# Optimization experiments

Hardware: AMD Instinct MI355X
Metric: run time of the kernel (lower is better)

## Reference

```python
import jax, jax.numpy as jnp
import numpy as np

D_IN = 1024
D_OUT = 1024
N_HEADS = 16
D_HEAD = D_OUT // N_HEADS


def setup_inputs() -> dict:
    key = jax.random.key(0)
    ks = jax.random.split(key, 6)
    s = 0.02
    return {
        "x": jax.random.normal(ks[0], (4, 2048, D_IN), dtype=jnp.float32),
        "wq": jax.random.normal(ks[1], (D_IN, D_OUT), dtype=jnp.float32) * s,
        "wk": jax.random.normal(ks[2], (D_IN, D_OUT), dtype=jnp.float32) * s,
        "wv": jax.random.normal(ks[3], (D_IN, D_OUT), dtype=jnp.float32) * s,
        "wo": jax.random.normal(ks[4], (D_OUT, D_OUT), dtype=jnp.float32) * s,
        "bo": jax.random.normal(ks[5], (D_OUT,), dtype=jnp.float32) * s,
    }


def reference(x, wq, wk, wv, wo, bo):
    B, T, _ = x.shape
    # QKV projections (no bias), split into heads: (B, H, T, Dh)
    def split_heads(t):
        return t.reshape(B, T, N_HEADS, D_HEAD).transpose(0, 2, 1, 3)
    q = split_heads(x @ wq)
    k = split_heads(x @ wk)
    v = split_heads(x @ wv)
    # attention scores (B, H, T, T), causal mask, scale by sqrt(d_head)
    scores = jnp.einsum("bhqd,bhkd->bhqk", q, k)
    causal = jnp.tril(jnp.ones((T, T), dtype=bool))
    scores = jnp.where(causal, scores, -jnp.inf)
    attn = jax.nn.softmax(scores / jnp.sqrt(jnp.float32(D_HEAD)), axis=-1)
    # dropout = 0.0 (eval) -> identity
    ctx = jnp.einsum("bhqk,bhkd->bhqd", attn, v)
    ctx = ctx.transpose(0, 2, 1, 3).reshape(B, T, D_OUT)
    return ctx @ wo + bo
```

## Files before the change

kernel.cpp:

```cpp
#include <hip/hip_runtime.h>
#include <stdint.h>


typedef unsigned short u16;
typedef __bf16 bf16x8 __attribute__((ext_vector_type(8)));
typedef float f32x4 __attribute__((ext_vector_type(4)));

__device__ __forceinline__ u16 f2bf(float f) {
  union { float f; unsigned u; } v; v.f = f;
  return (u16)((v.u + 0x7fffu + ((v.u >> 16) & 1u)) >> 16);
}

__device__ __forceinline__ void gl_lds16(const void* g, void* l) {
  __builtin_amdgcn_global_load_lds((__attribute__((address_space(1))) void*)g,
                                   (__attribute__((address_space(3))) void*)l,
                                   16, 0, 0);
}

__global__ __launch_bounds__(256) void conv_x_k(const float* __restrict__ x,
                                                u16* __restrict__ xb) {
  int i = (blockIdx.x * 256 + threadIdx.x) * 4;
  float4 v = *reinterpret_cast<const float4*>(x + i);
  ushort4 o;
  o.x = f2bf(v.x); o.y = f2bf(v.y); o.z = f2bf(v.z); o.w = f2bf(v.w);
  *reinterpret_cast<ushort4*>(xb + i) = o;
}

__global__ __launch_bounds__(256) void conv_w_k(const float* __restrict__ w0,
                                                const float* __restrict__ w1,
                                                const float* __restrict__ w2,
                                                const float* __restrict__ w3,
                                                u16* __restrict__ dst) {
  const float* src = blockIdx.z == 0 ? w0 : blockIdx.z == 1 ? w1
                   : blockIdx.z == 2 ? w2 : w3;
  u16* d = dst + (size_t)blockIdx.z * 1024 * 1024;
  __shared__ float tile[32][33];
  int n0 = blockIdx.x * 32, k0 = blockIdx.y * 32;
  int tx = threadIdx.x & 31, ty = threadIdx.x >> 5;
  #pragma unroll
  for (int r = 0; r < 32; r += 8)
    tile[ty + r][tx] = src[(k0 + ty + r) * 1024 + n0 + tx];
  __syncthreads();
  #pragma unroll
  for (int r = 0; r < 32; r += 8)
    d[(n0 + ty + r) * 1024 + k0 + tx] = f2bf(tile[tx][ty + r]);
}

__global__ __launch_bounds__(256) void gemm_qkv_k(const u16* __restrict__ A,
                                                  const u16* __restrict__ Wt,
                                                  u16* __restrict__ qw,
                                                  u16* __restrict__ kw,
                                                  u16* __restrict__ vtw) {
  __shared__ u16 As[128 * 32];
  __shared__ u16 Bs[128 * 32];
  const int tid = threadIdx.x;
  const int wave = tid >> 6, lane = tid & 63;
  const int quad = lane >> 4, l15 = lane & 15;
  const int m0 = blockIdx.x * 128;
  const int which = blockIdx.y >> 3;
  const int n0 = (blockIdx.y & 7) * 128;
  const u16* Bt = Wt + which * (1024 * 1024);
  const int waveM = (wave >> 1) * 64, waveN = (wave & 1) * 64;

  const f32x4 fz = {0.f, 0.f, 0.f, 0.f};
  f32x4 acc[4][4];
  #pragma unroll
  for (int i = 0; i < 4; i++)
    #pragma unroll
    for (int j = 0; j < 4; j++) acc[i][j] = fz;

  const int grow = tid >> 2, gc8 = (tid & 3) * 8;
  const u16* Ag = A + (m0 + grow) * 1024 + gc8;
  const u16* Bg = Bt + (n0 + grow) * 1024 + gc8;
  char* AsB = (char*)As + wave * 1024;
  char* BsB = (char*)Bs + wave * 1024;

  for (int k0 = 0; k0 < 1024; k0 += 32) {
    __syncthreads();
    gl_lds16(Ag + k0, AsB);
    gl_lds16(Ag + 65536 + k0, AsB + 4096);
    gl_lds16(Bg + k0, BsB);
    gl_lds16(Bg + 65536 + k0, BsB + 4096);
    __syncthreads();
    bf16x8 af[4], bf[4];
    #pragma unroll
    for (int mi = 0; mi < 4; mi++)
      af[mi] = *reinterpret_cast<const bf16x8*>(&As[(waveM + mi * 16 + l15) * 32 + quad * 8]);
    #pragma unroll
    for (int ni = 0; ni < 4; ni++)
      bf[ni] = *reinterpret_cast<const bf16x8*>(&Bs[(waveN + ni * 16 + l15) * 32 + quad * 8]);
    #pragma unroll
    for (int mi = 0; mi < 4; mi++)
      #pragma unroll
      for (int ni = 0; ni < 4; ni++)
        acc[mi][ni] = __builtin_amdgcn_mfma_f32_16x16x32_bf16(af[mi], bf[ni], acc[mi][ni], 0, 0, 0);
  }
  #pragma unroll
  for (int mi = 0; mi < 4; mi++) {
    #pragma unroll
    for (int r = 0; r < 4; r++) {
      int m = m0 + waveM + mi * 16 + quad * 4 + r;
      int b = m >> 11, t = m & 2047;
      #pragma unroll
      for (int ni = 0; ni < 4; ni++) {
        int n = n0 + waveN + ni * 16 + l15;
        int h = n >> 6, d = n & 63;
        float v = acc[mi][ni][r];
        if (which == 0)      qw[((b * 16 + h) * 2048 + t) * 64 + d] = f2bf(v * 0.125f);
        else if (which == 1) kw[((b * 16 + h) * 2048 + t) * 64 + d] = f2bf(v);
        else                 vtw[((b * 16 + h) * 64 + d) * 2048 + t] = f2bf(v);
      }
    }
  }
}

__global__ __launch_bounds__(256) void attn_k(const u16* __restrict__ Q,
                                              const u16* __restrict__ K,
                                              const u16* __restrict__ Vt,
                                              u16* __restrict__ ctx) {
  __shared__ u16 QPs[64 * 64];
  __shared__ u16 Ks[2][64 * 64];
  __shared__ u16 Vs[2][64 * 64];
  const int tid = threadIdx.x;
  const int wave = tid >> 6, lane = tid & 63;
  const int quad = lane >> 4, l15 = lane & 15;
  const int bh = blockIdx.x;
  const int qt = 31 - (int)blockIdx.y;
  const int b = bh >> 4, h = bh & 15;

  const u16* Qg = Q + (bh * 2048 + qt * 64) * 64;
  const u16* Kg = K + bh * (2048 * 64);
  const u16* Vg = Vt + bh * (64 * 2048);

  const int lrow = tid >> 3;
  const int lsw = ((tid & 7) ^ (lrow & 7)) * 8;

  gl_lds16(Qg + lrow * 64 + lsw, (char*)QPs + wave * 1024);
  gl_lds16(Qg + (32 + lrow) * 64 + lsw, (char*)QPs + wave * 1024 + 4096);
  {
    char* KsB = (char*)Ks[0] + wave * 1024;
    char* VsB = (char*)Vs[0] + wave * 1024;
    gl_lds16(Kg + lrow * 64 + lsw, KsB);
    gl_lds16(Kg + (32 + lrow) * 64 + lsw, KsB + 4096);
    gl_lds16(Vg + lrow * 2048 + lsw, VsB);
    gl_lds16(Vg + (32 + lrow) * 2048 + lsw, VsB + 4096);
  }

  bf16x8 onesb;
  #pragma unroll
  for (int i = 0; i < 8; i++) onesb[i] = (__bf16)1.0f;

  const f32x4 fz = {0.f, 0.f, 0.f, 0.f};
  f32x4 accO[4];
  f32x4 accL = fz;
  #pragma unroll
  for (int dt = 0; dt < 4; dt++) accO[dt] = fz;
  bf16x8 qf[2];

  #define SWZB(row, chunk) ((row) * 128 + (((chunk) ^ ((row) & 7)) << 4))

  for (int j = 0; j <= qt; j++) {
    const int cur = j & 1;
    __syncthreads();
    if (j < qt) {
      char* KsB = (char*)Ks[cur ^ 1] + wave * 1024;
      char* VsB = (char*)Vs[cur ^ 1] + wave * 1024;
      const int jr = (j + 1) * 64;
      gl_lds16(Kg + (jr + lrow) * 64 + lsw, KsB);
      gl_lds16(Kg + (jr + 32 + lrow) * 64 + lsw, KsB + 4096);
      gl_lds16(Vg + lrow * 2048 + jr + lsw, VsB);
      gl_lds16(Vg + (32 + lrow) * 2048 + jr + lsw, VsB + 4096);
    }
    if (j == 0) {
      #pragma unroll
      for (int kk = 0; kk < 2; kk++)
        qf[kk] = *reinterpret_cast<const bf16x8*>(
            (char*)QPs + SWZB(wave * 16 + l15, kk * 4 + quad));
    }

    f32x4 s[4];
    #pragma unroll
    for (int nt = 0; nt < 4; nt++) s[nt] = fz;
    #pragma unroll
    for (int kk = 0; kk < 2; kk++)
      #pragma unroll
      for (int nt = 0; nt < 4; nt++) {
        bf16x8 kf = *reinterpret_cast<const bf16x8*>(
            (char*)Ks[cur] + SWZB(nt * 16 + l15, kk * 4 + quad));
        s[nt] = __builtin_amdgcn_mfma_f32_16x16x32_bf16(qf[kk], kf, s[nt], 0, 0, 0);
      }

    if (j == qt) {
      #pragma unroll
      for (int nt = 0; nt < 4; nt++) {
        int col = nt * 16 + l15;
        int row0 = wave * 16 + quad * 4;
        #pragma unroll
        for (int r = 0; r < 4; r++)
          if (col > row0 + r) s[nt][r] = -1e30f;
      }
    }

    #pragma unroll
    for (int nt = 0; nt < 4; nt++)
      #pragma unroll
      for (int r = 0; r < 4; r++) {
        int prow = wave * 16 + quad * 4 + r;
        int pcol = nt * 16 + l15;
        int byte = prow * 128 + ((((pcol >> 3) ^ (prow & 7))) << 4) + (pcol & 7) * 2;
        *(u16*)((char*)QPs + byte) = f2bf(__expf(s[nt][r]));
      }
    __asm__ volatile("s_waitcnt lgkmcnt(0)" ::: "memory");

    #pragma unroll
    for (int kk = 0; kk < 2; kk++) {
      bf16x8 pf = *reinterpret_cast<const bf16x8*>(
          (char*)QPs + SWZB(wave * 16 + l15, kk * 4 + quad));
      accL = __builtin_amdgcn_mfma_f32_16x16x32_bf16(pf, onesb, accL, 0, 0, 0);
      #pragma unroll
      for (int dt = 0; dt < 4; dt++) {
        bf16x8 vf = *reinterpret_cast<const bf16x8*>(
            (char*)Vs[cur] + SWZB(dt * 16 + l15, kk * 4 + quad));
        accO[dt] = __builtin_amdgcn_mfma_f32_16x16x32_bf16(pf, vf, accO[dt], 0, 0, 0);
      }
    }
  }
  #undef SWZB

  float inv[4];
  #pragma unroll
  for (int r = 0; r < 4; r++) inv[r] = 1.0f / accL[r];
  const int trow = qt * 64 + wave * 16 + quad * 4;
  #pragma unroll
  for (int dt = 0; dt < 4; dt++)
    #pragma unroll
    for (int r = 0; r < 4; r++)
      ctx[(b * 2048 + trow + r) * 1024 + h * 64 + dt * 16 + l15] =
          f2bf(accO[dt][r] * inv[r]);
}

__global__ __launch_bounds__(256) void gemm_out_k(const u16* __restrict__ A,
                                                  const u16* __restrict__ Wt,
                                                  const float* __restrict__ bo,
                                                  float* __restrict__ out) {
  __shared__ u16 As[128 * 32];
  __shared__ u16 Bs[128 * 32];
  const int tid = threadIdx.x;
  const int wave = tid >> 6, lane = tid & 63;
  const int quad = lane >> 4, l15 = lane & 15;
  const int m0 = blockIdx.x * 128;
  const int n0 = blockIdx.y * 128;
  const int waveM = (wave >> 1) * 64, waveN = (wave & 1) * 64;

  const f32x4 fz = {0.f, 0.f, 0.f, 0.f};
  f32x4 acc[4][4];
  #pragma unroll
  for (int i = 0; i < 4; i++)
    #pragma unroll
    for (int j = 0; j < 4; j++) acc[i][j] = fz;

  const int grow = tid >> 2, gc8 = (tid & 3) * 8;
  const u16* Ag = A + (m0 + grow) * 1024 + gc8;
  const u16* Bg = Wt + (n0 + grow) * 1024 + gc8;
  char* AsB = (char*)As + wave * 1024;
  char* BsB = (char*)Bs + wave * 1024;

  for (int k0 = 0; k0 < 1024; k0 += 32) {
    __syncthreads();
    gl_lds16(Ag + k0, AsB);
    gl_lds16(Ag + 65536 + k0, AsB + 4096);
    gl_lds16(Bg + k0, BsB);
    gl_lds16(Bg + 65536 + k0, BsB + 4096);
    __syncthreads();
    bf16x8 af[4], bf[4];
    #pragma unroll
    for (int mi = 0; mi < 4; mi++)
      af[mi] = *reinterpret_cast<const bf16x8*>(&As[(waveM + mi * 16 + l15) * 32 + quad * 8]);
    #pragma unroll
    for (int ni = 0; ni < 4; ni++)
      bf[ni] = *reinterpret_cast<const bf16x8*>(&Bs[(waveN + ni * 16 + l15) * 32 + quad * 8]);
    #pragma unroll
    for (int mi = 0; mi < 4; mi++)
      #pragma unroll
      for (int ni = 0; ni < 4; ni++)
        acc[mi][ni] = __builtin_amdgcn_mfma_f32_16x16x32_bf16(af[mi], bf[ni], acc[mi][ni], 0, 0, 0);
  }
  float bias[4];
  #pragma unroll
  for (int ni = 0; ni < 4; ni++) bias[ni] = bo[n0 + waveN + ni * 16 + l15];
  #pragma unroll
  for (int mi = 0; mi < 4; mi++)
    #pragma unroll
    for (int r = 0; r < 4; r++) {
      int m = m0 + waveM + mi * 16 + quad * 4 + r;
      #pragma unroll
      for (int ni = 0; ni < 4; ni++) {
        int n = n0 + waveN + ni * 16 + l15;
        out[(size_t)m * 1024 + n] = acc[mi][ni][r] + bias[ni];
      }
    }
}

extern "C" void kernel_launch(void* const* d_in, const int* in_sizes, int n_in,
                              void* d_out, int out_size, void* d_ws, size_t ws_size,
                              hipStream_t stream) {
  const float* x  = (const float*)d_in[0];
  const float* wq = (const float*)d_in[1];
  const float* wk = (const float*)d_in[2];
  const float* wv = (const float*)d_in[3];
  const float* wo = (const float*)d_in[4];
  const float* bo = (const float*)d_in[5];
  float* out = (float*)d_out;
  char* ws = (char*)d_ws;

  u16* xb  = (u16*)(ws);
  u16* wt  = (u16*)(ws + 16777216);
  u16* qw  = (u16*)(ws + 25165824);
  u16* kw  = (u16*)(ws + 41943040);
  u16* vtw = (u16*)(ws + 58720256);

  conv_x_k<<<8192, 256, 0, stream>>>(x, xb);
  conv_w_k<<<dim3(32, 32, 4), 256, 0, stream>>>(wq, wk, wv, wo, wt);
  gemm_qkv_k<<<dim3(64, 24), 256, 0, stream>>>(xb, wt, qw, kw, vtw);
  attn_k<<<dim3(64, 32), 256, 0, stream>>>(qw, kw, vtw, xb );
  gemm_out_k<<<dim3(64, 8), 256, 0, stream>>>(xb, wt + 3 * 1024 * 1024, bo, out);
}
```

Baseline: 265.7 us.

## Double-buffer GEMM LDS tiles with XOR swizzle and coalesce V-transpose stores

Both projection GEMMs now keep two LDS stage buffers. The global-to-LDS load for the next K slice is issued right after a single barrier while MFMAs run on the current slice, which removes one barrier per iteration and overlaps load latency with compute. LDS rows are XOR-swizzled on the 16-byte chunk index, applied on both the global source offset and the fragment read, to reduce bank conflicts on fragment loads. The V output is transposed through LDS and written as contiguous 16-byte vectors along T instead of scattered 2-byte stores. The cost is doubled LDS per block (32 KB) and reliance on the barrier waiting for the async loads before the buffer is read.

```diff
diff --git a/kernel.cpp b/kernel.cpp
--- a/kernel.cpp
+++ b/kernel.cpp
@@ -46,13 +46,15 @@
     d[(n0 + ty + r) * 1024 + k0 + tx] = f2bf(tile[tx][ty + r]);
 }
 
+#define GSW(base, row, chunk) \
+  ((char*)(base) + (row) * 64 + ((((chunk) ^ (((row) >> 1) & 3))) << 4))
+
 __global__ __launch_bounds__(256) void gemm_qkv_k(const u16* __restrict__ A,
                                                   const u16* __restrict__ Wt,
                                                   u16* __restrict__ qw,
                                                   u16* __restrict__ kw,
                                                   u16* __restrict__ vtw) {
-  __shared__ u16 As[128 * 32];
-  __shared__ u16 Bs[128 * 32];
+  __shared__ u16 SM[16384];
   const int tid = threadIdx.x;
   const int wave = tid >> 6, lane = tid & 63;
   const int quad = lane >> 4, l15 = lane & 15;
@@ -69,47 +71,85 @@
     #pragma unroll
     for (int j = 0; j < 4; j++) acc[i][j] = fz;
 
-  const int grow = tid >> 2, gc8 = (tid & 3) * 8;
-  const u16* Ag = A + (m0 + grow) * 1024 + gc8;
-  const u16* Bg = Bt + (n0 + grow) * 1024 + gc8;
-  char* AsB = (char*)As + wave * 1024;
-  char* BsB = (char*)Bs + wave * 1024;
-
-  for (int k0 = 0; k0 < 1024; k0 += 32) {
-    __syncthreads();
-    gl_lds16(Ag + k0, AsB);
-    gl_lds16(Ag + 65536 + k0, AsB + 4096);
-    gl_lds16(Bg + k0, BsB);
-    gl_lds16(Bg + 65536 + k0, BsB + 4096);
-    __syncthreads();
+  const int grow = tid >> 2;
+  const int gsw8 = (((tid & 3) ^ ((grow >> 1) & 3)) * 8);
+  const u16* Ag = A + (m0 + grow) * 1024 + gsw8;
+  const u16* Bg = Bt + (n0 + grow) * 1024 + gsw8;
+
+  {
+    char* AsB = (char*)&SM[0] + wave * 1024;
+    char* BsB = (char*)&SM[8192] + wave * 1024;
+    gl_lds16(Ag, AsB);       gl_lds16(Ag + 65536, AsB + 4096);
+    gl_lds16(Bg, BsB);       gl_lds16(Bg + 65536, BsB + 4096);
+  }
+
+  for (int s = 0; s < 32; s++) {
+    const int cur = (s & 1) * 4096;
+    __syncthreads();
+    if (s < 31) {
+      const int k0 = (s + 1) * 32;
+      const int nxt = 4096 - cur;
+      char* AsB = (char*)&SM[nxt] + wave * 1024;
+      char* BsB = (char*)&SM[8192 + nxt] + wave * 1024;
+      gl_lds16(Ag + k0, AsB);      gl_lds16(Ag + 65536 + k0, AsB + 4096);
+      gl_lds16(Bg + k0, BsB);      gl_lds16(Bg + 65536 + k0, BsB + 4096);
+    }
     bf16x8 af[4], bf[4];
     #pragma unroll
     for (int mi = 0; mi < 4; mi++)
-      af[mi] = *reinterpret_cast<const bf16x8*>(&As[(waveM + mi * 16 + l15) * 32 + quad * 8]);
+      af[mi] = *reinterpret_cast<const bf16x8*>(GSW(&SM[cur], waveM + mi * 16 + l15, quad));
     #pragma unroll
     for (int ni = 0; ni < 4; ni++)
-      bf[ni] = *reinterpret_cast<const bf16x8*>(&Bs[(waveN + ni * 16 + l15) * 32 + quad * 8]);
+      bf[ni] = *reinterpret_cast<const bf16x8*>(GSW(&SM[8192 + cur], waveN + ni * 16 + l15, quad));
     #pragma unroll
     for (int mi = 0; mi < 4; mi++)
       #pragma unroll
       for (int ni = 0; ni < 4; ni++)
         acc[mi][ni] = __builtin_amdgcn_mfma_f32_16x16x32_bf16(af[mi], bf[ni], acc[mi][ni], 0, 0, 0);
   }
-  #pragma unroll
-  for (int mi = 0; mi < 4; mi++) {
-    #pragma unroll
-    for (int r = 0; r < 4; r++) {
-      int m = m0 + waveM + mi * 16 + quad * 4 + r;
-      int b = m >> 11, t = m & 2047;
-      #pragma unroll
-      for (int ni = 0; ni < 4; ni++) {
-        int n = n0 + waveN + ni * 16 + l15;
-        int h = n >> 6, d = n & 63;
-        float v = acc[mi][ni][r];
-        if (which == 0)      qw[((b * 16 + h) * 2048 + t) * 64 + d] = f2bf(v * 0.125f);
-        else if (which == 1) kw[((b * 16 + h) * 2048 + t) * 64 + d] = f2bf(v);
-        else                 vtw[((b * 16 + h) * 64 + d) * 2048 + t] = f2bf(v);
-      }
+
+  if (which != 2) {
+    #pragma unroll
+    for (int mi = 0; mi < 4; mi++) {
+      #pragma unroll
+      for (int r = 0; r < 4; r++) {
+        int m = m0 + waveM + mi * 16 + quad * 4 + r;
+        int b = m >> 11, t = m & 2047;
+        #pragma unroll
+        for (int ni = 0; ni < 4; ni++) {
+          int n = n0 + waveN + ni * 16 + l15;
+          int h = n >> 6, d = n & 63;
+          float v = acc[mi][ni][r];
+          if (which == 0) qw[((b * 16 + h) * 2048 + t) * 64 + d] = f2bf(v * 0.125f);
+          else            kw[((b * 16 + h) * 2048 + t) * 64 + d] = f2bf(v);
+        }
+      }
+    }
+  } else {
+    __syncthreads();
+    #pragma unroll
+    for (int mi = 0; mi < 4; mi++)
+      #pragma unroll
+      for (int r = 0; r < 4; r++) {
+        int ml = waveM + mi * 16 + quad * 4 + r;
+        #pragma unroll
+        for (int ni = 0; ni < 4; ni++) {
+          int nl = waveN + ni * 16 + l15;
+          int byte = nl * 256 + (((ml >> 3) ^ (nl & 7)) << 4) + (ml & 7) * 2;
+          *(u16*)((char*)SM + byte) = f2bf(acc[mi][ni][r]);
+        }
+      }
+    __syncthreads();
+    const int b = m0 >> 11, t0 = m0 & 2047;
+    #pragma unroll
+    for (int i = 0; i < 8; i++) {
+      int cid = tid + 256 * i;
+      int nl = cid >> 4, tc = cid & 15;
+      bf16x8 vv = *reinterpret_cast<const bf16x8*>(
+          (char*)SM + nl * 256 + ((tc ^ (nl & 7)) << 4));
+      int n = n0 + nl;
+      int h = n >> 6, d = n & 63;
+      *reinterpret_cast<bf16x8*>(vtw + (((b * 16 + h) * 64 + d) * 2048 + t0 + tc * 8)) = vv;
     }
   }
 }
@@ -243,8 +283,7 @@
                                                   const u16* __restrict__ Wt,
                                                   const float* __restrict__ bo,
                                                   float* __restrict__ out) {
-  __shared__ u16 As[128 * 32];
-  __shared__ u16 Bs[128 * 32];
+  __shared__ u16 SM[16384];
   const int tid = threadIdx.x;
   const int wave = tid >> 6, lane = tid & 63;
   const int quad = lane >> 4, l15 = lane & 15;
@@ -259,26 +298,36 @@
     #pragma unroll
     for (int j = 0; j < 4; j++) acc[i][j] = fz;
 
-  const int grow = tid >> 2, gc8 = (tid & 3) * 8;
-  const u16* Ag = A + (m0 + grow) * 1024 + gc8;
-  const u16* Bg = Wt + (n0 + grow) * 1024 + gc8;
-  char* AsB = (char*)As + wave * 1024;
-  char* BsB = (char*)Bs + wave * 1024;
-
-  for (int k0 = 0; k0 < 1024; k0 += 32) {
-    __syncthreads();
-    gl_lds16(Ag + k0, AsB);
-    gl_lds16(Ag + 65536 + k0, AsB + 4096);
-    gl_lds16(Bg + k0, BsB);
-    gl_lds16(Bg + 65536 + k0, BsB + 4096);
-    __syncthreads();
+  const int grow = tid >> 2;
+  const int gsw8 = (((tid & 3) ^ ((grow >> 1) & 3)) * 8);
+  const u16* Ag = A + (m0 + grow) * 1024 + gsw8;
+  const u16* Bg = Wt + (n0 + grow) * 1024 + gsw8;
+
+  {
+    char* AsB = (char*)&SM[0] + wave * 1024;
+    char* BsB = (char*)&SM[8192] + wave * 1024;
+    gl_lds16(Ag, AsB);       gl_lds16(Ag + 65536, AsB + 4096);
+    gl_lds16(Bg, BsB);       gl_lds16(Bg + 65536, BsB + 4096);
+  }
+
+  for (int s = 0; s < 32; s++) {
+    const int cur = (s & 1) * 4096;
+    __syncthreads();
+    if (s < 31) {
+      const int k0 = (s + 1) * 32;
+      const int nxt = 4096 - cur;
+      char* AsB = (char*)&SM[nxt] + wave * 1024;
+      char* BsB = (char*)&SM[8192 + nxt] + wave * 1024;
+      gl_lds16(Ag + k0, AsB);      gl_lds16(Ag + 65536 + k0, AsB + 4096);
+      gl_lds16(Bg + k0, BsB);      gl_lds16(Bg + 65536 + k0, BsB + 4096);
+    }
     bf16x8 af[4], bf[4];
     #pragma unroll
     for (int mi = 0; mi < 4; mi++)
-      af[mi] = *reinterpret_cast<const bf16x8*>(&As[(waveM + mi * 16 + l15) * 32 + quad * 8]);
+      af[mi] = *reinterpret_cast<const bf16x8*>(GSW(&SM[cur], waveM + mi * 16 + l15, quad));
     #pragma unroll
     for (int ni = 0; ni < 4; ni++)
-      bf[ni] = *reinterpret_cast<const bf16x8*>(&Bs[(waveN + ni * 16 + l15) * 32 + quad * 8]);
+      bf[ni] = *reinterpret_cast<const bf16x8*>(GSW(&SM[8192 + cur], waveN + ni * 16 + l15, quad));
     #pragma unroll
     for (int mi = 0; mi < 4; mi++)
       #pragma unroll
```

Measured after the change: 254.5 us. 4.2% less time.
